# Optimization experiments

Measured on AMD Instinct MI355X. Metric: run time of the kernel, lower is better.

## Reference

```python
import jax, jax.numpy as jnp
import numpy as np

EPS = 1e-8  # torch F.cosine_similarity clamps norms at eps=1e-8


def setup_inputs() -> dict:
    key = jax.random.key(0)
    N, M, D = 1024, 20, 768  # speakers, utterances/speaker, embed dim
    embeddings = jax.random.normal(key, (N, M, D), dtype=jnp.float32)
    w = jnp.asarray(10.0, dtype=jnp.float32)  # init_w
    b = jnp.asarray(-5.0, dtype=jnp.float32)  # init_b
    return {"embeddings": embeddings, "w": w, "b": b}


def reference(embeddings, w, b):
    N, M, D = embeddings.shape
    centroids = embeddings.mean(axis=1)  # [N, D]
    # cosine similarity as one fused GEMM on normalized vectors
    e = embeddings / jnp.maximum(
        jnp.linalg.norm(embeddings, axis=-1, keepdims=True), EPS)
    c = centroids / jnp.maximum(
        jnp.linalg.norm(centroids, axis=-1, keepdims=True), EPS)
    # sim[j, i, m] = cos(e[i, m], centroid[j])  -- matches the torch loop/stack
    sim = jnp.einsum('imd,jd->jim', e, c)
    logits = w * sim + b  # [N_j, N_i, M]
    # torch: view(N*N, M).transpose(0,1).reshape(-1, N)
    #   => row index r = m*N + j, column i
    logits = jnp.transpose(logits, (2, 0, 1)).reshape(N * M, N)
    # torch labels: arange(N) expanded over M -> labels[r] = r // M
    labels = jnp.repeat(jnp.arange(N), M)
    logp = jax.nn.log_softmax(logits, axis=-1)
    loss = -jnp.mean(logp[jnp.arange(N * M), labels])
    return loss
```

## Files before the change

kernel.cpp:

```cpp
#include <hip/hip_runtime.h>
#include <hip/hip_bf16.h>
#include <cstdint>

#define N_SPK 1024
#define M_UTT 20
#define D_DIM 768
#define NM_ROWS (N_SPK * M_UTT)

static constexpr float EPS = 1e-8f;

typedef __attribute__((ext_vector_type(8))) short short8;
typedef __attribute__((ext_vector_type(4))) float floatx4;

__device__ __forceinline__ void load16_to_lds(const void* g, void* l) {
    __builtin_amdgcn_global_load_lds(
        (const __attribute__((address_space(1))) uint32_t*)g,
        (__attribute__((address_space(3))) uint32_t*)l, 16, 0, 0);
}

__device__ __forceinline__ unsigned short bf16bits(float x) {
    __hip_bfloat16 h = __float2bfloat16(x);
    return *(unsigned short*)&h;
}

__device__ __forceinline__ float wave_sum(float v) {
    #pragma unroll
    for (int o = 32; o > 0; o >>= 1) v += __shfl_xor(v, o);
    return v;
}

__global__ __launch_bounds__(384) void prep_kernel(const float* __restrict__ emb,
                                                   __hip_bfloat16* __restrict__ ehat,
                                                   __hip_bfloat16* __restrict__ chat,
                                                   int* __restrict__ ctr,
                                                   float* __restrict__ accum) {
    const int i = blockIdx.x;
    const int t = threadIdx.x;
    const int wave = t >> 6, lane = t & 63;

    if (i == 0 && t == 0) { *ctr = 0; *accum = 0.f; }

    const float2* src = (const float2*)(emb + (size_t)i * M_UTT * D_DIM);

    float2 v[M_UTT];
    float ss[M_UTT];
    float2 cen = {0.f, 0.f};
    #pragma unroll
    for (int m = 0; m < M_UTT; ++m) {
        const float2 x = src[m * 384 + t];
        v[m] = x;
        ss[m] = x.x * x.x + x.y * x.y;
        cen.x += x.x; cen.y += x.y;
    }
    cen.x *= (1.f / M_UTT); cen.y *= (1.f / M_UTT);
    float css = cen.x * cen.x + cen.y * cen.y;

    __shared__ float red[M_UTT + 1][6];
    #pragma unroll
    for (int m = 0; m < M_UTT; ++m) {
        const float s = wave_sum(ss[m]);
        if (lane == 0) red[m][wave] = s;
    }
    {
        const float s = wave_sum(css);
        if (lane == 0) red[M_UTT][wave] = s;
    }
    __syncthreads();

    #pragma unroll
    for (int m = 0; m < M_UTT; ++m) {
        const float tot = red[m][0] + red[m][1] + red[m][2] +
                          red[m][3] + red[m][4] + red[m][5];
        const float rn = 1.0f / fmaxf(sqrtf(tot), EPS);
        ushort2 o;
        o.x = bf16bits(v[m].x * rn); o.y = bf16bits(v[m].y * rn);
        *(ushort2*)((unsigned short*)ehat + ((size_t)(m * N_SPK + i)) * D_DIM + 2 * t) = o;
    }
    {
        const float tot = red[M_UTT][0] + red[M_UTT][1] + red[M_UTT][2] +
                          red[M_UTT][3] + red[M_UTT][4] + red[M_UTT][5];
        const float rn = 1.0f / fmaxf(sqrtf(tot), EPS);
        ushort2 o;
        o.x = bf16bits(cen.x * rn); o.y = bf16bits(cen.y * rn);
        *(ushort2*)((unsigned short*)chat + (size_t)i * D_DIM + 2 * t) = o;
    }
}

__global__ __launch_bounds__(128) void gemm_fused_kernel(
        const __hip_bfloat16* __restrict__ ehat,
        const __hip_bfloat16* __restrict__ chat,
        const float* __restrict__ wp,
        float* __restrict__ Psum,
        float* __restrict__ T) {
    __shared__ __hip_bfloat16 As[128 * 32];
    __shared__ __hip_bfloat16 Bs[64 * 32];
    __shared__ float red[2][64];

    const int t = threadIdx.x;
    const int lane = t & 63;
    const int wid = t >> 6;
    const int c = lane & 15;
    const int quad = lane >> 4;

    const int xcd = blockIdx.x & 7;
    const int idx = blockIdx.x >> 3;
    const int bu  = xcd * 20 + (idx >> 4);
    const int bj  = idx & 15;
    const int m   = bu >> 3;
    const int rb  = bu & 7;
    const int u0  = bu * 128;
    const int j0  = bj * 64;

    const short* Ag = (const short*)ehat + (size_t)u0 * D_DIM;
    const short* Bg = (const short*)chat + (size_t)j0 * D_DIM;

    floatx4 acc[4][4] = {};

    for (int k0 = 0; k0 < D_DIM; k0 += 32) {
        #pragma unroll
        for (int s = 0; s < 4; ++s) {
            const int ci  = s * 128 + t;
            const int row = ci >> 2;
            const int q   = (ci & 3) ^ ((row >> 1) & 3);
            load16_to_lds(Ag + (size_t)row * D_DIM + k0 + q * 8, (short*)As + ci * 8);
        }
        #pragma unroll
        for (int s = 0; s < 2; ++s) {
            const int ci  = s * 128 + t;
            const int row = ci >> 2;
            const int q   = (ci & 3) ^ ((row >> 1) & 3);
            load16_to_lds(Bg + (size_t)row * D_DIM + k0 + q * 8, (short*)Bs + ci * 8);
        }
        __syncthreads();

        short8 af[4], bf[4];
        #pragma unroll
        for (int it = 0; it < 4; ++it) {
            const int r = wid * 64 + it * 16 + c;
            const int slot = r * 4 + (quad ^ ((r >> 1) & 3));
            af[it] = *(const short8*)((const short*)As + slot * 8);
        }
        #pragma unroll
        for (int jt = 0; jt < 4; ++jt) {
            const int r = jt * 16 + c;
            const int slot = r * 4 + (quad ^ ((r >> 1) & 3));
            bf[jt] = *(const short8*)((const short*)Bs + slot * 8);
        }

        #pragma unroll
        for (int it = 0; it < 4; ++it)
            #pragma unroll
            for (int jt = 0; jt < 4; ++jt)
                acc[it][jt] = __builtin_amdgcn_mfma_f32_16x16x32_bf16(af[it], bf[jt], acc[it][jt], 0, 0, 0);
        __syncthreads();
    }

    const float w = wp[0];

    #pragma unroll
    for (int jt = 0; jt < 4; ++jt) {
        float sm = 0.f;
        #pragma unroll
        for (int it = 0; it < 4; ++it)
            #pragma unroll
            for (int r = 0; r < 4; ++r)
                sm += __expf(w * (acc[it][jt][r] - 1.0f));
        sm += __shfl_xor(sm, 16);
        sm += __shfl_xor(sm, 32);
        if (quad == 0) red[wid][jt * 16 + c] = sm;
    }

    #pragma unroll
    for (int it = 0; it < 4; ++it) {
        #pragma unroll
        for (int jt = 0; jt < 4; ++jt) {
            const int col = j0 + jt * 16 + c;
            const int g = m * N_SPK + col;
            const int istar = g / M_UTT;
            const int rbase = rb * 128 + wid * 64 + it * 16 + quad * 4;
            #pragma unroll
            for (int r = 0; r < 4; ++r) {
                if (rbase + r == istar) T[g] = acc[it][jt][r];
            }
        }
    }

    __syncthreads();
    if (wid == 0) {
        const int cc = lane;
        Psum[(m * 8 + rb) * N_SPK + j0 + cc] = red[0][cc] + red[1][cc];
    }
}

__global__ void combine_kernel(const float* __restrict__ Psum,
                               const float* __restrict__ T,
                               const float* __restrict__ wp,
                               int* __restrict__ ctr,
                               float* __restrict__ accum,
                               float* __restrict__ out) {
    const int p = blockIdx.x * 256 + threadIdx.x;
    const int m = p >> 10;
    const int j = p & 1023;
    const float w = wp[0];

    float S = 0.f;
    #pragma unroll
    for (int rb = 0; rb < 8; ++rb)
        S += Psum[(m * 8 + rb) * N_SPK + j];
    const float term = w * (T[p] - 1.0f) - __logf(S);

    __shared__ float red[256];
    red[threadIdx.x] = term;
    __syncthreads();
    for (int o = 128; o > 0; o >>= 1) {
        if (threadIdx.x < o) red[threadIdx.x] += red[threadIdx.x + o];
        __syncthreads();
    }
    if (threadIdx.x == 0) {
        atomicAdd(accum, red[0]);
        __threadfence();
        const int old = atomicAdd(ctr, 1);
        if (old == 79) {
            const float a = atomicAdd(accum, 0.0f);
            out[0] = -a / (float)NM_ROWS;
        }
    }
}

extern "C" void kernel_launch(void* const* d_in, const int* in_sizes, int n_in,
                              void* d_out, int out_size, void* d_ws, size_t ws_size,
                              hipStream_t stream) {
    const float* emb = (const float*)d_in[0];
    const float* wp  = (const float*)d_in[1];
    float* out = (float*)d_out;

    char* ws = (char*)d_ws;
    __hip_bfloat16* ehat = (__hip_bfloat16*)(ws);
    __hip_bfloat16* chat = (__hip_bfloat16*)(ws + 31457280);
    float* Psum  = (float*)(ws + 33030144);
    float* T     = (float*)(ws + 33685504);
    int*   ctr   = (int*)  (ws + 33767424);
    float* accum = (float*)(ws + 33767428);

    prep_kernel<<<dim3(N_SPK), dim3(384), 0, stream>>>(emb, ehat, chat, ctr, accum);
    gemm_fused_kernel<<<dim3(2560), dim3(128), 0, stream>>>(ehat, chat, wp, Psum, T);
    combine_kernel<<<dim3(80), dim3(256), 0, stream>>>(Psum, T, wp, ctr, accum, out);
}
```

Measured before the change: 161.1 us.

## Use single-wave GEMM blocks with waitcnt-based sync instead of barriers

Shrinks the GEMM block from two waves over a 128-row tile to one wave over a 64-row tile, doubling the grid and the number of partial-sum rows. Because only one wave owns the LDS tile, __syncthreads is replaced by explicit s_waitcnt on vmem and lgkm counters. The next K-slice loads are issued right after the MFMAs. Partial sums are written straight to global memory without the LDS cross-wave reduction, and the combine kernel now sums 16 partials instead of 8. This trades barrier cost for more blocks, twice the B-tile reloads per output, and reliance on manual waitcnt encodings being correct.

```diff
diff --git a/kernel.cpp b/kernel.cpp
--- a/kernel.cpp
+++ b/kernel.cpp
@@ -8,6 +8,9 @@
 #define NM_ROWS (N_SPK * M_UTT)
 
 static constexpr float EPS = 1e-8f;
+
+#define WAIT_VM0   0x0F70
+#define WAIT_LGKM0 0xC07F
 
 typedef __attribute__((ext_vector_type(8))) short short8;
 typedef __attribute__((ext_vector_type(4))) float floatx4;
@@ -86,57 +89,55 @@
     }
 }
 
-__global__ __launch_bounds__(128) void gemm_fused_kernel(
+__global__ __launch_bounds__(64) void gemm_fused_kernel(
         const __hip_bfloat16* __restrict__ ehat,
         const __hip_bfloat16* __restrict__ chat,
         const float* __restrict__ wp,
         float* __restrict__ Psum,
         float* __restrict__ T) {
-    __shared__ __hip_bfloat16 As[128 * 32];
+    __shared__ __hip_bfloat16 As[64 * 32];
     __shared__ __hip_bfloat16 Bs[64 * 32];
-    __shared__ float red[2][64];
-
-    const int t = threadIdx.x;
-    const int lane = t & 63;
-    const int wid = t >> 6;
+
+    const int lane = threadIdx.x;
     const int c = lane & 15;
     const int quad = lane >> 4;
 
     const int xcd = blockIdx.x & 7;
     const int idx = blockIdx.x >> 3;
-    const int bu  = xcd * 20 + (idx >> 4);
+    const int bu  = xcd * 40 + (idx >> 4);
     const int bj  = idx & 15;
-    const int m   = bu >> 3;
-    const int rb  = bu & 7;
-    const int u0  = bu * 128;
+    const int m   = bu >> 4;
+    const int rb  = bu & 15;
+    const int u0  = bu * 64;
     const int j0  = bj * 64;
 
     const short* Ag = (const short*)ehat + (size_t)u0 * D_DIM;
     const short* Bg = (const short*)chat + (size_t)j0 * D_DIM;
 
+    int arow[4], aq[4];
+    #pragma unroll
+    for (int s = 0; s < 4; ++s) {
+        const int ci  = s * 64 + lane;
+        arow[s] = ci >> 2;
+        aq[s]   = (ci & 3) ^ ((arow[s] >> 1) & 3);
+    }
+
     floatx4 acc[4][4] = {};
 
-    for (int k0 = 0; k0 < D_DIM; k0 += 32) {
-        #pragma unroll
-        for (int s = 0; s < 4; ++s) {
-            const int ci  = s * 128 + t;
-            const int row = ci >> 2;
-            const int q   = (ci & 3) ^ ((row >> 1) & 3);
-            load16_to_lds(Ag + (size_t)row * D_DIM + k0 + q * 8, (short*)As + ci * 8);
-        }
-        #pragma unroll
-        for (int s = 0; s < 2; ++s) {
-            const int ci  = s * 128 + t;
-            const int row = ci >> 2;
-            const int q   = (ci & 3) ^ ((row >> 1) & 3);
-            load16_to_lds(Bg + (size_t)row * D_DIM + k0 + q * 8, (short*)Bs + ci * 8);
-        }
-        __syncthreads();
+    #pragma unroll
+    for (int s = 0; s < 4; ++s) {
+        const int ci = s * 64 + lane;
+        load16_to_lds(Ag + (size_t)arow[s] * D_DIM + aq[s] * 8, (short*)As + ci * 8);
+        load16_to_lds(Bg + (size_t)arow[s] * D_DIM + aq[s] * 8, (short*)Bs + ci * 8);
+    }
+
+    for (int it24 = 0; it24 < 24; ++it24) {
+        __builtin_amdgcn_s_waitcnt(WAIT_VM0);
 
         short8 af[4], bf[4];
         #pragma unroll
         for (int it = 0; it < 4; ++it) {
-            const int r = wid * 64 + it * 16 + c;
+            const int r = it * 16 + c;
             const int slot = r * 4 + (quad ^ ((r >> 1) & 3));
             af[it] = *(const short8*)((const short*)As + slot * 8);
         }
@@ -152,7 +153,17 @@
             #pragma unroll
             for (int jt = 0; jt < 4; ++jt)
                 acc[it][jt] = __builtin_amdgcn_mfma_f32_16x16x32_bf16(af[it], bf[jt], acc[it][jt], 0, 0, 0);
-        __syncthreads();
+
+        if (it24 < 23) {
+            const int k0 = (it24 + 1) * 32;
+            __builtin_amdgcn_s_waitcnt(WAIT_LGKM0);
+            #pragma unroll
+            for (int s = 0; s < 4; ++s) {
+                const int ci = s * 64 + lane;
+                load16_to_lds(Ag + (size_t)arow[s] * D_DIM + k0 + aq[s] * 8, (short*)As + ci * 8);
+                load16_to_lds(Bg + (size_t)arow[s] * D_DIM + k0 + aq[s] * 8, (short*)Bs + ci * 8);
+            }
+        }
     }
 
     const float w = wp[0];
@@ -167,7 +178,7 @@
                 sm += __expf(w * (acc[it][jt][r] - 1.0f));
         sm += __shfl_xor(sm, 16);
         sm += __shfl_xor(sm, 32);
-        if (quad == 0) red[wid][jt * 16 + c] = sm;
+        if (quad == 0) Psum[(size_t)bu * N_SPK + j0 + jt * 16 + c] = sm;
     }
 
     #pragma unroll
@@ -177,18 +188,12 @@
             const int col = j0 + jt * 16 + c;
             const int g = m * N_SPK + col;
             const int istar = g / M_UTT;
-            const int rbase = rb * 128 + wid * 64 + it * 16 + quad * 4;
+            const int rloc = rb * 64 + it * 16 + quad * 4;
             #pragma unroll
             for (int r = 0; r < 4; ++r) {
-                if (rbase + r == istar) T[g] = acc[it][jt][r];
+                if (rloc + r == istar) T[g] = acc[it][jt][r];
             }
         }
-    }
-
-    __syncthreads();
-    if (wid == 0) {
-        const int cc = lane;
-        Psum[(m * 8 + rb) * N_SPK + j0 + cc] = red[0][cc] + red[1][cc];
     }
 }
 
@@ -205,8 +210,8 @@
 
     float S = 0.f;
     #pragma unroll
-    for (int rb = 0; rb < 8; ++rb)
-        S += Psum[(m * 8 + rb) * N_SPK + j];
+    for (int rb = 0; rb < 16; ++rb)
+        S += Psum[(size_t)(m * 16 + rb) * N_SPK + j];
     const float term = w * (T[p] - 1.0f) - __logf(S);
 
     __shared__ float red[256];
@@ -238,11 +243,11 @@
     __hip_bfloat16* ehat = (__hip_bfloat16*)(ws);
     __hip_bfloat16* chat = (__hip_bfloat16*)(ws + 31457280);
     float* Psum  = (float*)(ws + 33030144);
-    float* T     = (float*)(ws + 33685504);
-    int*   ctr   = (int*)  (ws + 33767424);
-    float* accum = (float*)(ws + 33767428);
+    float* T     = (float*)(ws + 34340864);
+    int*   ctr   = (int*)  (ws + 34422784);
+    float* accum = (float*)(ws + 34422788);
 
     prep_kernel<<<dim3(N_SPK), dim3(384), 0, stream>>>(emb, ehat, chat, ctr, accum);
-    gemm_fused_kernel<<<dim3(2560), dim3(128), 0, stream>>>(ehat, chat, wp, Psum, T);
+    gemm_fused_kernel<<<dim3(320 * 16), dim3(64), 0, stream>>>(ehat, chat, wp, Psum, T);
     combine_kernel<<<dim3(80), dim3(256), 0, stream>>>(Psum, T, wp, ctr, accum, out);
 }
```

Measured after the change: 165.7 us. 1.03x slower.
